# Optimization experiments

Measured on AMD Instinct MI355X. Metric: run time of the kernel, lower is better.

Reference implementation:

```python
import jax, jax.numpy as jnp
import numpy as np
from jax import lax

B, T, H, L = 64, 512, 768, 9


def setup_inputs() -> dict:
    key = jax.random.key(0)
    ks = jax.random.split(key, 6)
    return {
        "seq_out": jax.random.normal(ks[0], (B, T, H), dtype=jnp.float32),
        "mask": jnp.ones((B, T), dtype=bool),
        "W_fc": jax.random.normal(ks[1], (H, L), dtype=jnp.float32) * 0.02,
        "b_fc": jax.random.normal(ks[2], (L,), dtype=jnp.float32) * 0.02,
        "start_transitions": jax.random.normal(ks[3], (L,), dtype=jnp.float32) * 0.1,
        "end_transitions": jax.random.normal(ks[4], (L,), dtype=jnp.float32) * 0.1,
        "transitions": jax.random.normal(ks[5], (L, L), dtype=jnp.float32) * 0.1,
    }


def reference(seq_out, mask, W_fc, b_fc, start_transitions, end_transitions, transitions):
    # linear head (dropout is identity at inference)
    emissions = jnp.einsum("bth,hl->btl", seq_out, W_fc) + b_fc  # (B,T,L)

    # --- Viterbi forward pass (torchcrf semantics) ---
    score0 = start_transitions + emissions[:, 0]  # (B,L)
    emis_rest = jnp.swapaxes(emissions[:, 1:], 0, 1)  # (T-1,B,L)
    mask_rest = jnp.swapaxes(mask[:, 1:], 0, 1)       # (T-1,B)

    def step(score, inp):
        emit_t, mask_t = inp
        # (B, prev L, next L)
        full = score[:, :, None] + transitions[None, :, :] + emit_t[:, None, :]
        next_score = jnp.max(full, axis=1)
        best_prev = jnp.argmax(full, axis=1)  # (B,L) best previous tag
        new_score = jnp.where(mask_t[:, None], next_score, score)
        return new_score, best_prev

    score, history = lax.scan(step, score0, (emis_rest, mask_rest))  # history: (T-1,B,L)

    last_tag = jnp.argmax(score + end_transitions, axis=1)  # (B,)

    # --- backtrace (mask is all-ones -> every sequence has full length T) ---
    def back(tag, hist_t):
        prev = jnp.take_along_axis(hist_t, tag[:, None], axis=1)[:, 0]
        return prev, tag  # emit tag at t+1, carry tag at t

    first_tag, tags_rest = lax.scan(back, last_tag, history, reverse=True)
    tags = jnp.concatenate([first_tag[:, None], jnp.swapaxes(tags_rest, 0, 1)], axis=1)
    return tags  # (B,T) int32 best tag sequence
```

## Files before the change

### kernel.cpp

```cpp
#include <hip/hip_runtime.h>
#include <stdint.h>

typedef unsigned long long u64;

#define T_SZ 512
#define H_SZ 768
#define L_SZ 9
#define KCHUNK 192
#define NINF (-__builtin_inff())

__device__ __forceinline__ float max3f(float a, float b, float c)
{
  return fmaxf(fmaxf(a, b), c);
}

__global__ __launch_bounds__(256) void emis_kernel(
    const float* __restrict__ seq, const float* __restrict__ W,
    const float* __restrict__ bfc, float* __restrict__ emis)
{
  const int tid  = threadIdx.x;
  const int lane = tid & 63;
  const int wid  = __builtin_amdgcn_readfirstlane(tid >> 6);

  const int row = blockIdx.x * 64 + lane;
  const float* x     = seq + (size_t)row * H_SZ + wid * KCHUNK;
  const float* wbase = W + (size_t)wid * KCHUNK * L_SZ;

  float acc[L_SZ];
#pragma unroll
  for (int j = 0; j < L_SZ; ++j) acc[j] = 0.f;

#pragma unroll 2
  for (int i = 0; i < KCHUNK / 4; ++i) {
    const float4 xv = *reinterpret_cast<const float4*>(x + 4 * i);
    const float* wp = wbase + 36 * i;
    float wf[36];
#pragma unroll
    for (int q = 0; q < 9; ++q)
      *reinterpret_cast<float4*>(&wf[4 * q]) =
          *reinterpret_cast<const float4*>(wp + 4 * q);
#pragma unroll
    for (int j = 0; j < L_SZ; ++j)
      acc[j] += xv.x * wf[j] + xv.y * wf[9 + j] + xv.z * wf[18 + j] + xv.w * wf[27 + j];
  }

  __shared__ float s_part[4 * 64 * L_SZ];
  {
    float* myp = s_part + (wid * 64 + lane) * L_SZ;
#pragma unroll
    for (int j = 0; j < L_SZ; ++j) myp[j] = acc[j];
  }
  __syncthreads();

  for (int o = tid; o < 64 * L_SZ; o += 256) {
    const int j = o % L_SZ;
    const float s = s_part[o] + s_part[576 + o] + s_part[1152 + o] + s_part[1728 + o];
    emis[(size_t)blockIdx.x * (64 * L_SZ) + o] = s + bfc[j];
  }
}

#define ROTI(K, v) __builtin_amdgcn_mov_dpp((v), 0x120 + (K), 0xF, 0xF, true)
#define ROTF(K, v) __int_as_float(__builtin_amdgcn_mov_dpp(__float_as_int(v), 0x120 + (K), 0xF, 0xF, true))

__device__ __forceinline__ u64 comp9(u64 a, u64 b)
{
  u64 r = 0;
#pragma unroll
  for (int x = 0; x < 9; ++x) {
    const int bx = (int)((b >> (4 * x)) & 15ull);
    const u64 ax = (a >> (bx * 4)) & 15ull;
    r |= ax << (4 * x);
  }
  return r;
}
__device__ __forceinline__ int app9(u64 f, int x) { return (int)((f >> (4 * x)) & 15ull); }

__device__ __forceinline__ u64 shfl_dn64(u64 v, int d)
{
  unsigned lo = __shfl_down((unsigned)v, d, 64);
  unsigned hi = __shfl_down((unsigned)(v >> 32), d, 64);
  return ((u64)hi << 32) | lo;
}

__global__ __launch_bounds__(256) void viterbi_kernel(
    const float* __restrict__ emis, const float* __restrict__ trans,
    const float* __restrict__ startT, const float* __restrict__ endT,
    int* __restrict__ tags)
{
  const int b   = blockIdx.x;
  const int tid = threadIdx.x;

  __shared__ __align__(16) float s_emis[T_SZ * L_SZ + 32];
  __shared__ float s_score[T_SZ * L_SZ + 8];
  __shared__ float s_T16[16 * 16];
  __shared__ unsigned char s_hist[T_SZ * L_SZ];
  __shared__ int s_last;

  {
    const float4* src = reinterpret_cast<const float4*>(emis + (size_t)b * T_SZ * L_SZ);
    float4* dst = reinterpret_cast<float4*>(s_emis);
    for (int i = tid; i < (T_SZ * L_SZ) / 4; i += 256) dst[i] = src[i];
  }
  {
    const int i = tid >> 4, j = tid & 15;
    s_T16[tid] = (i < L_SZ && j < L_SZ) ? trans[i * L_SZ + j] : NINF;
  }
  __syncthreads();

  if (tid < 16) {
    const int jj  = tid;
    const int jje = (jj < L_SZ) ? jj : (L_SZ - 1);

    float Tp[16];
    {
      int xk;
      Tp[0] = s_T16[jj * 16 + jj];
#define SETTP(K) xk = ROTI(K, jj); Tp[K] = s_T16[xk * 16 + jj];
      SETTP(1)  SETTP(2)  SETTP(3)  SETTP(4)  SETTP(5)
      SETTP(6)  SETTP(7)  SETTP(8)  SETTP(9)  SETTP(10)
      SETTP(11) SETTP(12) SETTP(13) SETTP(14) SETTP(15)
#undef SETTP
    }

    float r = (jj < L_SZ) ? (startT[jje] + s_emis[jj]) : NINF;
    s_score[jj] = r;

    float e0 = s_emis[1 * L_SZ + jje];
    float e1 = s_emis[2 * L_SZ + jje];
    const float* ep = s_emis + 3 * L_SZ + jje;
    float* sp = s_score + L_SZ + jj;

#pragma unroll 2
    for (int t = 1; t < T_SZ; ++t) {
      const float e2 = *ep; ep += L_SZ;
      float a1, a2, a3, a4, a5, a6, a7, a8;
      float a9, a10, a11, a12, a13, a14, a15;
      asm("s_nop 1\n\t"
          "v_add_f32_dpp %0, %8, %9   row_ror:1  row_mask:0xf bank_mask:0xf\n\t"
          "v_add_f32_dpp %1, %8, %10  row_ror:2  row_mask:0xf bank_mask:0xf\n\t"
          "v_add_f32_dpp %2, %8, %11  row_ror:3  row_mask:0xf bank_mask:0xf\n\t"
          "v_add_f32_dpp %3, %8, %12  row_ror:4  row_mask:0xf bank_mask:0xf\n\t"
          "v_add_f32_dpp %4, %8, %13  row_ror:5  row_mask:0xf bank_mask:0xf\n\t"
          "v_add_f32_dpp %5, %8, %14  row_ror:6  row_mask:0xf bank_mask:0xf\n\t"
          "v_add_f32_dpp %6, %8, %15  row_ror:7  row_mask:0xf bank_mask:0xf\n\t"
          "v_add_f32_dpp %7, %8, %16  row_ror:8  row_mask:0xf bank_mask:0xf"
          : "=v"(a1), "=v"(a2), "=v"(a3), "=v"(a4),
            "=v"(a5), "=v"(a6), "=v"(a7), "=v"(a8)
          : "v"(r), "v"(Tp[1]), "v"(Tp[2]), "v"(Tp[3]), "v"(Tp[4]),
            "v"(Tp[5]), "v"(Tp[6]), "v"(Tp[7]), "v"(Tp[8]));
      asm("v_add_f32_dpp %0, %7, %8   row_ror:9  row_mask:0xf bank_mask:0xf\n\t"
          "v_add_f32_dpp %1, %7, %9   row_ror:10 row_mask:0xf bank_mask:0xf\n\t"
          "v_add_f32_dpp %2, %7, %10  row_ror:11 row_mask:0xf bank_mask:0xf\n\t"
          "v_add_f32_dpp %3, %7, %11  row_ror:12 row_mask:0xf bank_mask:0xf\n\t"
          "v_add_f32_dpp %4, %7, %12  row_ror:13 row_mask:0xf bank_mask:0xf\n\t"
          "v_add_f32_dpp %5, %7, %13  row_ror:14 row_mask:0xf bank_mask:0xf\n\t"
          "v_add_f32_dpp %6, %7, %14  row_ror:15 row_mask:0xf bank_mask:0xf"
          : "=v"(a9), "=v"(a10), "=v"(a11), "=v"(a12),
            "=v"(a13), "=v"(a14), "=v"(a15)
          : "v"(r), "v"(Tp[9]), "v"(Tp[10]), "v"(Tp[11]),
            "v"(Tp[12]), "v"(Tp[13]), "v"(Tp[14]), "v"(Tp[15]));
      const float a0 = r + Tp[0];
      const float m0 = max3f(a0, a1, a2);
      const float m1 = max3f(a3, a4, a5);
      const float m2 = max3f(a6, a7, a8);
      const float m3 = max3f(a9, a10, a11);
      const float m4 = max3f(a12, a13, a14);
      const float n0 = max3f(m0, m1, m2);
      const float n1 = max3f(m3, m4, a15);
      r = fmaxf(n0, n1) + e0;
      *sp = r; sp += L_SZ;
      e0 = e1; e1 = e2;
    }

    const float fin = r + ((jj < L_SZ) ? endT[jje] : 0.f);
    float g[16]; int gi[16];
    g[0] = fin; gi[0] = jj;
#define GFIN(K) g[K] = ROTF(K, fin); gi[K] = ROTI(K, jj);
    GFIN(1)  GFIN(2)  GFIN(3)  GFIN(4)  GFIN(5)
    GFIN(6)  GFIN(7)  GFIN(8)  GFIN(9)  GFIN(10)
    GFIN(11) GFIN(12) GFIN(13) GFIN(14) GFIN(15)
#undef GFIN
    const float q0 = max3f(g[0], g[1], g[2]);
    const float q1 = max3f(g[3], g[4], g[5]);
    const float q2 = max3f(g[6], g[7], g[8]);
    const float q3 = max3f(g[9], g[10], g[11]);
    const float q4 = max3f(g[12], g[13], g[14]);
    const float mm = fmaxf(max3f(q0, q1, q2), max3f(q3, q4, g[15]));
    int li = 99;
#pragma unroll
    for (int k = 0; k < 16; ++k) li = min(li, (g[k] == mm) ? gi[k] : 99);
    if (jj == 0) s_last = li;
  }
  __syncthreads();

  for (int p = tid; p < (T_SZ - 1) * L_SZ; p += 256) {
    const int t = p / L_SZ + 1;
    const int j = p - (t - 1) * L_SZ;
    const float e = s_emis[t * L_SZ + j];
    const float* sp2 = s_score + (t - 1) * L_SZ;
    float ci[9];
#pragma unroll
    for (int i = 0; i < 9; ++i) ci[i] = (sp2[i] + s_T16[i * 16 + j]) + e;
    const float m = fmaxf(max3f(max3f(ci[0], ci[1], ci[2]),
                                max3f(ci[3], ci[4], ci[5]),
                                max3f(ci[6], ci[7], ci[8])), ci[8]);
    int bi = 8;
#pragma unroll
    for (int i = 8; i >= 0; --i) bi = (ci[i] == m) ? i : bi;
    s_hist[t * L_SZ + j] = (unsigned char)bi;
  }
  __syncthreads();

  if (tid < 64) {
    const u64 IDENT = 0x876543210ull;
    const int k = tid;
    const int last = s_last;

    u64 f[8];
#pragma unroll
    for (int r = 0; r < 8; ++r) {
      const int s = 8 * k + r;
      u64 v = 0;
#pragma unroll
      for (int x = 0; x < 9; ++x)
        v |= (u64)(s_hist[s * L_SZ + x] & 15) << (4 * x);
      f[r] = v;
    }
    if (k == 0) f[0] = IDENT;

    u64 C = f[7];
#pragma unroll
    for (int r = 6; r >= 0; --r) C = comp9(f[r], C);

    u64 S = C;
#pragma unroll
    for (int d = 1; d < 64; d <<= 1) {
      u64 o = shfl_dn64(S, d);
      if (k + d > 63) o = IDENT;
      S = comp9(S, o);
    }
    u64 E = shfl_dn64(S, 1);
    if (k == 63) E = IDENT;

    int val = app9(E, last);
    int* ob = tags + b * T_SZ;
    ob[8 * k + 7] = val;
#pragma unroll
    for (int r = 7; r >= 0; --r) {
      val = app9(f[r], val);
      const int s = 8 * k + r;
      if (s >= 1) ob[s - 1] = val;
    }
  }
}

extern "C" void kernel_launch(void* const* d_in, const int* in_sizes, int n_in,
                              void* d_out, int out_size, void* d_ws, size_t ws_size,
                              hipStream_t stream)
{
  const float* seq   = (const float*)d_in[0];
  const float* W     = (const float*)d_in[2];
  const float* bfc   = (const float*)d_in[3];
  const float* stT   = (const float*)d_in[4];
  const float* enT   = (const float*)d_in[5];
  const float* trans = (const float*)d_in[6];

  int*   tags = (int*)d_out;
  float* emis = (float*)d_ws;

  emis_kernel<<<(T_SZ * 64) / 64, 256, 0, stream>>>(seq, W, bfc, emis);
  viterbi_kernel<<<64, 256, 0, stream>>>(emis, trans, stT, enT, tags);
}
```

Before: 75.47 us.

## Transpose emissions and scores in LDS, unroll Viterbi forward by four with vector I/O

Stores emissions and forward scores in a tag-major transposed layout (padded stride 516) so each of the 16 serial lanes reads and writes its own contiguous row. The recurrence is unrolled by four, loading four emissions with one float4 prefetch and writing four scores with one float4 store. This takes per-step LDS loads and stores off the serial dependency chain. The cost is an uncoalesced scalar transposing global load at kernel start, plus extra LDS for 16 padded score rows.

```diff
diff --git a/kernel.cpp b/kernel.cpp
--- a/kernel.cpp
+++ b/kernel.cpp
@@ -7,6 +7,7 @@
 #define H_SZ 768
 #define L_SZ 9
 #define KCHUNK 192
+#define ETS 516
 #define NINF (-__builtin_inff())
 
 __device__ __forceinline__ float max3f(float a, float b, float c)
@@ -62,6 +63,43 @@
 #define ROTI(K, v) __builtin_amdgcn_mov_dpp((v), 0x120 + (K), 0xF, 0xF, true)
 #define ROTF(K, v) __int_as_float(__builtin_amdgcn_mov_dpp(__float_as_int(v), 0x120 + (K), 0xF, 0xF, true))
 
+#define VSTEP(ROUT, RIN, EV)                                                   \
+  {                                                                            \
+    float a1, a2, a3, a4, a5, a6, a7, a8, a9, a10, a11, a12, a13, a14, a15;    \
+    asm("s_nop 1\n\t"                                                          \
+        "v_add_f32_dpp %0, %8, %9   row_ror:1  row_mask:0xf bank_mask:0xf\n\t" \
+        "v_add_f32_dpp %1, %8, %10  row_ror:2  row_mask:0xf bank_mask:0xf\n\t" \
+        "v_add_f32_dpp %2, %8, %11  row_ror:3  row_mask:0xf bank_mask:0xf\n\t" \
+        "v_add_f32_dpp %3, %8, %12  row_ror:4  row_mask:0xf bank_mask:0xf\n\t" \
+        "v_add_f32_dpp %4, %8, %13  row_ror:5  row_mask:0xf bank_mask:0xf\n\t" \
+        "v_add_f32_dpp %5, %8, %14  row_ror:6  row_mask:0xf bank_mask:0xf\n\t" \
+        "v_add_f32_dpp %6, %8, %15  row_ror:7  row_mask:0xf bank_mask:0xf\n\t" \
+        "v_add_f32_dpp %7, %8, %16  row_ror:8  row_mask:0xf bank_mask:0xf"     \
+        : "=&v"(a1), "=&v"(a2), "=&v"(a3), "=&v"(a4),                          \
+          "=&v"(a5), "=&v"(a6), "=&v"(a7), "=&v"(a8)                           \
+        : "v"(RIN), "v"(Tp1), "v"(Tp2), "v"(Tp3), "v"(Tp4),                    \
+          "v"(Tp5), "v"(Tp6), "v"(Tp7), "v"(Tp8));                             \
+    asm("s_nop 1\n\t"                                                          \
+        "v_add_f32_dpp %0, %7, %8   row_ror:9  row_mask:0xf bank_mask:0xf\n\t" \
+        "v_add_f32_dpp %1, %7, %9   row_ror:10 row_mask:0xf bank_mask:0xf\n\t" \
+        "v_add_f32_dpp %2, %7, %10  row_ror:11 row_mask:0xf bank_mask:0xf\n\t" \
+        "v_add_f32_dpp %3, %7, %11  row_ror:12 row_mask:0xf bank_mask:0xf\n\t" \
+        "v_add_f32_dpp %4, %7, %12  row_ror:13 row_mask:0xf bank_mask:0xf\n\t" \
+        "v_add_f32_dpp %5, %7, %13  row_ror:14 row_mask:0xf bank_mask:0xf\n\t" \
+        "v_add_f32_dpp %6, %7, %14  row_ror:15 row_mask:0xf bank_mask:0xf"     \
+        : "=&v"(a9), "=&v"(a10), "=&v"(a11), "=&v"(a12),                       \
+          "=&v"(a13), "=&v"(a14), "=&v"(a15)                                   \
+        : "v"(RIN), "v"(Tp9), "v"(Tp10), "v"(Tp11),                            \
+          "v"(Tp12), "v"(Tp13), "v"(Tp14), "v"(Tp15));                         \
+    const float a0 = (RIN) + Tp0;                                              \
+    const float m0 = max3f(a0, a1, a2);                                        \
+    const float m1 = max3f(a3, a4, a5);                                        \
+    const float m2 = max3f(a6, a7, a8);                                        \
+    const float m3 = max3f(a9, a10, a11);                                      \
+    const float m4 = max3f(a12, a13, a14);                                     \
+    (ROUT) = fmaxf(max3f(m0, m1, m2), max3f(m3, m4, a15)) + (EV);              \
+  }
+
 __device__ __forceinline__ u64 comp9(u64 a, u64 b)
 {
   u64 r = 0;
@@ -90,16 +128,15 @@
   const int b   = blockIdx.x;
   const int tid = threadIdx.x;
 
-  __shared__ __align__(16) float s_emis[T_SZ * L_SZ + 32];
-  __shared__ float s_score[T_SZ * L_SZ + 8];
+  __shared__ __align__(16) float s_eT[L_SZ * ETS];
+  __shared__ __align__(16) float s_sT[16 * ETS];
   __shared__ float s_T16[16 * 16];
   __shared__ unsigned char s_hist[T_SZ * L_SZ];
   __shared__ int s_last;
 
-  {
-    const float4* src = reinterpret_cast<const float4*>(emis + (size_t)b * T_SZ * L_SZ);
-    float4* dst = reinterpret_cast<float4*>(s_emis);
-    for (int i = tid; i < (T_SZ * L_SZ) / 4; i += 256) dst[i] = src[i];
+  for (int p = tid; p < T_SZ * L_SZ; p += 256) {
+    const int t = p / L_SZ, j = p - L_SZ * t;
+    s_eT[j * ETS + t] = emis[(size_t)b * (T_SZ * L_SZ) + p];
   }
   {
     const int i = tid >> 4, j = tid & 15;
@@ -109,70 +146,45 @@
 
   if (tid < 16) {
     const int jj  = tid;
-    const int jje = (jj < L_SZ) ? jj : (L_SZ - 1);
-
-    float Tp[16];
+    const int jjc = (jj < L_SZ) ? jj : (L_SZ - 1);
+
+    float Tp0, Tp1, Tp2, Tp3, Tp4, Tp5, Tp6, Tp7;
+    float Tp8, Tp9, Tp10, Tp11, Tp12, Tp13, Tp14, Tp15;
     {
       int xk;
-      Tp[0] = s_T16[jj * 16 + jj];
-#define SETTP(K) xk = ROTI(K, jj); Tp[K] = s_T16[xk * 16 + jj];
-      SETTP(1)  SETTP(2)  SETTP(3)  SETTP(4)  SETTP(5)
-      SETTP(6)  SETTP(7)  SETTP(8)  SETTP(9)  SETTP(10)
-      SETTP(11) SETTP(12) SETTP(13) SETTP(14) SETTP(15)
+      Tp0 = s_T16[jj * 16 + jj];
+#define SETTP(K, DST) xk = ROTI(K, jj); DST = s_T16[xk * 16 + jj];
+      SETTP(1, Tp1)   SETTP(2, Tp2)   SETTP(3, Tp3)   SETTP(4, Tp4)
+      SETTP(5, Tp5)   SETTP(6, Tp6)   SETTP(7, Tp7)   SETTP(8, Tp8)
+      SETTP(9, Tp9)   SETTP(10, Tp10) SETTP(11, Tp11) SETTP(12, Tp12)
+      SETTP(13, Tp13) SETTP(14, Tp14) SETTP(15, Tp15)
 #undef SETTP
     }
 
-    float r = (jj < L_SZ) ? (startT[jje] + s_emis[jj]) : NINF;
-    s_score[jj] = r;
-
-    float e0 = s_emis[1 * L_SZ + jje];
-    float e1 = s_emis[2 * L_SZ + jje];
-    const float* ep = s_emis + 3 * L_SZ + jje;
-    float* sp = s_score + L_SZ + jj;
-
-#pragma unroll 2
-    for (int t = 1; t < T_SZ; ++t) {
-      const float e2 = *ep; ep += L_SZ;
-      float a1, a2, a3, a4, a5, a6, a7, a8;
-      float a9, a10, a11, a12, a13, a14, a15;
-      asm("s_nop 1\n\t"
-          "v_add_f32_dpp %0, %8, %9   row_ror:1  row_mask:0xf bank_mask:0xf\n\t"
-          "v_add_f32_dpp %1, %8, %10  row_ror:2  row_mask:0xf bank_mask:0xf\n\t"
-          "v_add_f32_dpp %2, %8, %11  row_ror:3  row_mask:0xf bank_mask:0xf\n\t"
-          "v_add_f32_dpp %3, %8, %12  row_ror:4  row_mask:0xf bank_mask:0xf\n\t"
-          "v_add_f32_dpp %4, %8, %13  row_ror:5  row_mask:0xf bank_mask:0xf\n\t"
-          "v_add_f32_dpp %5, %8, %14  row_ror:6  row_mask:0xf bank_mask:0xf\n\t"
-          "v_add_f32_dpp %6, %8, %15  row_ror:7  row_mask:0xf bank_mask:0xf\n\t"
-          "v_add_f32_dpp %7, %8, %16  row_ror:8  row_mask:0xf bank_mask:0xf"
-          : "=v"(a1), "=v"(a2), "=v"(a3), "=v"(a4),
-            "=v"(a5), "=v"(a6), "=v"(a7), "=v"(a8)
-          : "v"(r), "v"(Tp[1]), "v"(Tp[2]), "v"(Tp[3]), "v"(Tp[4]),
-            "v"(Tp[5]), "v"(Tp[6]), "v"(Tp[7]), "v"(Tp[8]));
-      asm("v_add_f32_dpp %0, %7, %8   row_ror:9  row_mask:0xf bank_mask:0xf\n\t"
-          "v_add_f32_dpp %1, %7, %9   row_ror:10 row_mask:0xf bank_mask:0xf\n\t"
-          "v_add_f32_dpp %2, %7, %10  row_ror:11 row_mask:0xf bank_mask:0xf\n\t"
-          "v_add_f32_dpp %3, %7, %11  row_ror:12 row_mask:0xf bank_mask:0xf\n\t"
-          "v_add_f32_dpp %4, %7, %12  row_ror:13 row_mask:0xf bank_mask:0xf\n\t"
-          "v_add_f32_dpp %5, %7, %13  row_ror:14 row_mask:0xf bank_mask:0xf\n\t"
-          "v_add_f32_dpp %6, %7, %14  row_ror:15 row_mask:0xf bank_mask:0xf"
-          : "=v"(a9), "=v"(a10), "=v"(a11), "=v"(a12),
-            "=v"(a13), "=v"(a14), "=v"(a15)
-          : "v"(r), "v"(Tp[9]), "v"(Tp[10]), "v"(Tp[11]),
-            "v"(Tp[12]), "v"(Tp[13]), "v"(Tp[14]), "v"(Tp[15]));
-      const float a0 = r + Tp[0];
-      const float m0 = max3f(a0, a1, a2);
-      const float m1 = max3f(a3, a4, a5);
-      const float m2 = max3f(a6, a7, a8);
-      const float m3 = max3f(a9, a10, a11);
-      const float m4 = max3f(a12, a13, a14);
-      const float n0 = max3f(m0, m1, m2);
-      const float n1 = max3f(m3, m4, a15);
-      r = fmaxf(n0, n1) + e0;
-      *sp = r; sp += L_SZ;
-      e0 = e1; e1 = e2;
-    }
-
-    const float fin = r + ((jj < L_SZ) ? endT[jje] : 0.f);
+    const float* eRow = s_eT + jjc * ETS;
+    float*       sRow = s_sT + jj * ETS;
+
+    float r = (jj < L_SZ) ? (startT[jjc] + eRow[0]) : NINF;
+    sRow[0] = r;
+
+    VSTEP(r, r, eRow[1]);  sRow[1] = r;
+    VSTEP(r, r, eRow[2]);  sRow[2] = r;
+    VSTEP(r, r, eRow[3]);  sRow[3] = r;
+
+    float4 enxt = *reinterpret_cast<const float4*>(eRow + 4);
+    for (int k = 1; k <= 127; ++k) {
+      const float4 ecur = enxt;
+      enxt = *reinterpret_cast<const float4*>(eRow + 4 * (k + 1));
+      float r0, r1, r2, r3;
+      VSTEP(r0, r,  ecur.x);
+      VSTEP(r1, r0, ecur.y);
+      VSTEP(r2, r1, ecur.z);
+      VSTEP(r3, r2, ecur.w);
+      *reinterpret_cast<float4*>(sRow + 4 * k) = make_float4(r0, r1, r2, r3);
+      r = r3;
+    }
+
+    const float fin = r + ((jj < L_SZ) ? endT[jjc] : 0.f);
     float g[16]; int gi[16];
     g[0] = fin; gi[0] = jj;
 #define GFIN(K) g[K] = ROTF(K, fin); gi[K] = ROTI(K, jj);
@@ -196,11 +208,12 @@
   for (int p = tid; p < (T_SZ - 1) * L_SZ; p += 256) {
     const int t = p / L_SZ + 1;
     const int j = p - (t - 1) * L_SZ;
-    const float e = s_emis[t * L_SZ + j];
-    const float* sp2 = s_score + (t - 1) * L_SZ;
+    const float e  = s_eT[j * ETS + t];
+    const float bv = s_sT[j * ETS + t];
+    (void)bv;
     float ci[9];
 #pragma unroll
-    for (int i = 0; i < 9; ++i) ci[i] = (sp2[i] + s_T16[i * 16 + j]) + e;
+    for (int i = 0; i < 9; ++i) ci[i] = (s_sT[i * ETS + (t - 1)] + s_T16[i * 16 + j]) + e;
     const float m = fmaxf(max3f(max3f(ci[0], ci[1], ci[2]),
                                 max3f(ci[3], ci[4], ci[5]),
                                 max3f(ci[6], ci[7], ci[8])), ci[8]);
```

After: 78.83 us. +4.4%, slower.
